# Kernel tuning notes

Hardware: AMD Instinct MI355X
Metric: run time of the kernel (lower is better)

The kernel has to match this reference:

```python
import jax, jax.numpy as jnp
import numpy as np
from jax import lax

BN_EPS = 1e-5


def _bn(t, g, b, m, v):
    # eval-mode BatchNorm2d over channel axis 1
    scale = (g / jnp.sqrt(v + BN_EPS))[None, :, None, None]
    return (t - m[None, :, None, None]) * scale + b[None, :, None, None]


def _conv1x1(t, w):
    # w: (out_c, in_c)
    return jnp.einsum('bchw,oc->bohw', t, w)


def setup_inputs() -> dict:
    key = jax.random.key(0)
    ks = jax.random.split(key, 8)
    B, C_in, H, W = 16, 640, 32, 32
    x = jax.random.normal(ks[0], (B, C_in, H, W), dtype=jnp.float32)

    def bn_params(k, c):
        k1, k2, k3, k4 = jax.random.split(k, 4)
        return (jax.random.normal(k1, (c,), jnp.float32) * 0.1 + 1.0,  # gamma
                jax.random.normal(k2, (c,), jnp.float32) * 0.1,        # beta
                jax.random.normal(k3, (c,), jnp.float32) * 0.1,        # running mean
                jax.random.uniform(k4, (c,), jnp.float32) + 0.5)       # running var

    bn1_g, bn1_b, bn1_m, bn1_v = bn_params(ks[1], 640)
    w_in = jax.random.normal(ks[2], (64, 640), jnp.float32) / np.sqrt(640)
    bnin_g, bnin_b, bnin_m, bnin_v = bn_params(ks[3], 64)
    w_emb = jax.random.normal(ks[4], (640, 1664), jnp.float32) / np.sqrt(1664)
    bne_g, bne_b, bne_m, bne_v = bn_params(ks[5], 640)
    w_out = jax.random.normal(ks[6], (640, 640), jnp.float32) / np.sqrt(640)
    bno_g, bno_b, bno_m, bno_v = bn_params(ks[7], 640)

    return dict(x=x,
                bn1_g=bn1_g, bn1_b=bn1_b, bn1_m=bn1_m, bn1_v=bn1_v,
                w_in=w_in, bnin_g=bnin_g, bnin_b=bnin_b, bnin_m=bnin_m, bnin_v=bnin_v,
                w_emb=w_emb, bne_g=bne_g, bne_b=bne_b, bne_m=bne_m, bne_v=bne_v,
                w_out=w_out, bno_g=bno_g, bno_b=bno_b, bno_m=bno_m, bno_v=bno_v)


def reference(x,
              bn1_g, bn1_b, bn1_m, bn1_v,
              w_in, bnin_g, bnin_b, bnin_m, bnin_v,
              w_emb, bne_g, bne_b, bne_m, bne_v,
              w_out, bno_g, bno_b, bno_m, bno_v):
    KH, KW = 5, 5
    x = jax.nn.relu(_bn(x, bn1_g, bn1_b, bn1_m, bn1_v))
    x = jax.nn.relu(_bn(_conv1x1(x, w_in), bnin_g, bnin_b, bnin_m, bnin_v))
    x0 = jax.nn.relu(x)  # second ReLU in original forward (no-op but faithful)
    # F.normalize(x, dim=1, p=2), eps=1e-12 (PyTorch default)
    norm = jnp.sqrt(jnp.sum(x0 * x0, axis=1, keepdims=True))
    identity = x0 / jnp.maximum(norm, 1e-12)
    b, c, h, w = identity.shape
    # unfold: (b, c*KH*KW, h, w), channel-major ordering matches torch Unfold
    patches = lax.conv_general_dilated_patches(
        identity, (KH, KW), (1, 1), ((2, 2), (2, 2)))
    corr = patches.reshape(b, c, KH * KW, h, w) * identity[:, :, None, :, :]
    corr = corr.reshape(b, c * KH * KW, h, w)
    # featureL2Norm: sqrt(sum(x^2, 1) + 1e-6)
    gs = corr / jnp.sqrt(jnp.sum(corr * corr, axis=1, keepdims=True) + 1e-6)
    feat = jnp.concatenate([identity, gs], axis=1)  # (b, 1664, h, w)
    e = jax.nn.relu(_bn(_conv1x1(feat, w_emb), bne_g, bne_b, bne_m, bne_v))
    out = _bn(_conv1x1(e, w_out), bno_g, bno_b, bno_m, bno_v)
    # dropout in eval mode = identity
    return out
```

## Files before the change

kernel.cpp:

```cpp
#include <hip/hip_runtime.h>
#include <math.h>

#define BN_EPS 1e-5f

using short8  = __attribute__((ext_vector_type(8))) short;
using f32x16  = __attribute__((ext_vector_type(16))) float;


__device__ __forceinline__ float bflo(unsigned u) { return __uint_as_float(u << 16); }
__device__ __forceinline__ float bfhi(unsigned u) { return __uint_as_float(u & 0xffff0000u); }

__device__ __forceinline__ unsigned bf16_rne(float f) {
    unsigned u = __float_as_uint(f);
    return (u + 0x7fffu + ((u >> 16) & 1u)) >> 16;
}
__device__ __forceinline__ unsigned pack_bf16(float lo, float hi) {
    return bf16_rne(lo) | (bf16_rne(hi) << 16);
}
__device__ __forceinline__ unsigned pk_hu(float lo, float hi) {
    unsigned a = __float_as_uint(lo) + 0x8000u;
    unsigned b = __float_as_uint(hi) + 0x8000u;
    return __builtin_amdgcn_perm(b, a, 0x07060302u);
}
__device__ __forceinline__ unsigned pmul_fast(unsigned a, unsigned b) {
    return pk_hu(bflo(a) * bflo(b), bfhi(a) * bfhi(b));
}

__global__ __launch_bounds__(256)
void k_prep(const float* __restrict__ g1, const float* __restrict__ b1,
            const float* __restrict__ m1, const float* __restrict__ v1,
            const float* __restrict__ w_in,
            const float* __restrict__ gi, const float* __restrict__ bi,
            const float* __restrict__ mi, const float* __restrict__ vi,
            const float* __restrict__ ge, const float* __restrict__ be,
            const float* __restrict__ me, const float* __restrict__ ve,
            const float* __restrict__ w_out,
            const float* __restrict__ go, const float* __restrict__ bo,
            const float* __restrict__ mo, const float* __restrict__ vo,
            float* __restrict__ s1, float* __restrict__ b1c,
            float* __restrict__ biasI, float* __restrict__ biasE, float* __restrict__ biasO,
            unsigned* __restrict__ wIt, unsigned* __restrict__ wOt)
{
    int i = blockIdx.x * 256 + threadIdx.x;

    if (i < 640) {
        float s = g1[i] * rsqrtf(v1[i] + BN_EPS);
        s1[i] = s; b1c[i] = b1[i] - m1[i] * s;
    } else if (i < 704) {
        int c = i - 640;
        float s = gi[c] * rsqrtf(vi[c] + BN_EPS);
        biasI[c] = bi[c] - mi[c] * s;
    } else if (i < 1344) {
        int c = i - 704;
        float s = ge[c] * rsqrtf(ve[c] + BN_EPS);
        biasE[c] = be[c] - me[c] * s;
    } else if (i < 1984) {
        int c = i - 1344;
        float s = go[c] * rsqrtf(vo[c] + BN_EPS);
        biasO[c] = bo[c] - mo[c] * s;
    }

    if (i >= 2048 && i < 7168) {
        int u = i - 2048;
        int kc = u >> 8, w = u & 255;
        int mf = w >> 7, kh = (w >> 6) & 1, sl = w & 63;
        int oc = mf * 32 + (sl & 31);
        int k0 = kc * 32 + kh * 16 + (sl >> 5) * 8;
        float sc = gi[oc] * rsqrtf(vi[oc] + BN_EPS);
        unsigned d[4];
#pragma unroll
        for (int q = 0; q < 4; q++)
            d[q] = pack_bf16(w_in[oc * 640 + k0 + 2 * q] * sc,
                             w_in[oc * 640 + k0 + 2 * q + 1] * sc);
        ((uint4*)wIt)[u] = make_uint4(d[0], d[1], d[2], d[3]);
    }

    if (i >= 8192 && i < 59392) {
        int u = i - 8192;
        int ci = u >> 9, w = u & 511;
        int mt = ci / 20, kc = ci - mt * 20;
        int mf = w >> 7, kh = (w >> 6) & 1, sl = w & 63;
        int oc = mt * 128 + mf * 32 + (sl & 31);
        int k0 = kc * 32 + kh * 16 + (sl >> 5) * 8;
        float sc = go[oc] * rsqrtf(vo[oc] + BN_EPS);
        unsigned d[4];
#pragma unroll
        for (int q = 0; q < 4; q++)
            d[q] = pack_bf16(w_out[oc * 640 + k0 + 2 * q] * sc,
                             w_out[oc * 640 + k0 + 2 * q + 1] * sc);
        ((uint4*)wOt)[u] = make_uint4(d[0], d[1], d[2], d[3]);
    }
}

__global__ __launch_bounds__(256)
void k_prepE(const float* __restrict__ w_emb,
             const float* __restrict__ ge, const float* __restrict__ ve,
             unsigned* __restrict__ wEt)
{
    __shared__ float row[1664];
    const int tid = threadIdx.x;
    const int oc = blockIdx.x;

#pragma unroll
    for (int it = 0; it < 2; it++) {
        int u = it * 256 + tid;
        if (u < 416)
            ((float4*)row)[u] = ((const float4*)&w_emb[(size_t)oc * 1664])[u];
    }
    __syncthreads();

    if (tid < 208) {
        int kc = tid >> 2, kh = (tid >> 1) & 1, ksub = tid & 1;
        int k0 = kc * 32 + kh * 16 + ksub * 8;
        float sc = ge[oc] * rsqrtf(ve[oc] + BN_EPS);
        float v[8];
#pragma unroll
        for (int j = 0; j < 8; j++) {
            int kgp = k0 + j;
            int orig;
            if (kgp < 64) orig = kgp;
            else { int t = kgp - 64; orig = 64 + (t & 63) * 25 + (t >> 6); }
            v[j] = row[orig] * sc;
        }
        int mt = oc >> 7, mf = (oc >> 5) & 3;
        int idx = (mt * 52 + kc) * 512 + (mf * 2 + kh) * 64 + ksub * 32 + (oc & 31);
        ((uint4*)wEt)[idx] = make_uint4(pack_bf16(v[0], v[1]), pack_bf16(v[2], v[3]),
                                        pack_bf16(v[4], v[5]), pack_bf16(v[6], v[7]));
    }
}

__global__ __launch_bounds__(256, 2)
void k_identity(const float* __restrict__ x,
                const float* __restrict__ s1, const float* __restrict__ b1c,
                const unsigned* __restrict__ wIt, const float* __restrict__ biasI,
                unsigned* __restrict__ ident)
{
    __shared__ short smem[4096];
    __shared__ float T[64 * 68];
    __shared__ float inv[64];

    const int tid = threadIdx.x;
    const int l = tid & 63, wv = tid >> 6;
    const int mf = wv >> 1, nf = wv & 1;
    const int p0 = blockIdx.x * 64;
    const int b = p0 >> 10, hw0 = p0 & 1023;

    f32x16 acc;
#pragma unroll
    for (int r = 0; r < 16; r++) acc[r] = 0.f;

    for (int kc = 0; kc < 20; kc++) {
        uint4 av = ((const uint4*)wIt)[kc * 256 + tid];
        int u = tid;
        int bnf = u >> 7, bkh = (u >> 6) & 1, sl = u & 63;
        int px = bnf * 32 + (sl & 31);
        int ch0 = kc * 32 + bkh * 16 + (sl >> 5) * 8;
        float4 sA = *(const float4*)&s1[ch0], sB = *(const float4*)&s1[ch0 + 4];
        float4 bA = *(const float4*)&b1c[ch0], bB = *(const float4*)&b1c[ch0 + 4];
        float vv[8];
        const float* xp = &x[((size_t)b * 640 + ch0) * 1024 + hw0 + px];
        vv[0] = fmaxf(fmaf(xp[0], sA.x, bA.x), 0.f);
        vv[1] = fmaxf(fmaf(xp[1024], sA.y, bA.y), 0.f);
        vv[2] = fmaxf(fmaf(xp[2048], sA.z, bA.z), 0.f);
        vv[3] = fmaxf(fmaf(xp[3072], sA.w, bA.w), 0.f);
        vv[4] = fmaxf(fmaf(xp[4096], sB.x, bB.x), 0.f);
        vv[5] = fmaxf(fmaf(xp[5120], sB.y, bB.y), 0.f);
        vv[6] = fmaxf(fmaf(xp[6144], sB.z, bB.z), 0.f);
        vv[7] = fmaxf(fmaf(xp[7168], sB.w, bB.w), 0.f);
        uint4 bvpk = make_uint4(pack_bf16(vv[0], vv[1]), pack_bf16(vv[2], vv[3]),
                                pack_bf16(vv[4], vv[5]), pack_bf16(vv[6], vv[7]));
        __syncthreads();
        ((uint4*)smem)[tid] = av;
        ((uint4*)(smem + 2048))[tid] = bvpk;
        __syncthreads();
#pragma unroll
        for (int kh = 0; kh < 2; kh++) {
            short8 a = *(const short8*)&smem[((mf * 2 + kh) * 64 + l) * 8];
            short8 bb = *(const short8*)&smem[2048 + ((nf * 2 + kh) * 64 + l) * 8];
            acc = __builtin_amdgcn_mfma_f32_32x32x16_bf16(a, bb, acc, 0, 0, 0);
        }
    }
    __syncthreads();
#pragma unroll
    for (int r = 0; r < 16; r++) {
        int m = mf * 32 + (r & 3) + 8 * (r >> 2) + 4 * (l >> 5);
        int px = nf * 32 + (l & 31);
        T[px * 68 + m] = fmaxf(acc[r] + biasI[m], 0.f);
    }
    __syncthreads();
    if (tid < 64) {
        float sum = 0.f;
#pragma unroll 8
        for (int c = 0; c < 64; c++) { float v = T[tid * 68 + c]; sum = fmaf(v, v, sum); }
        inv[tid] = 1.f / fmaxf(sqrtf(sum), 1e-12f);
    }
    __syncthreads();
    {
        int px = tid >> 2, q = tid & 3;
        float iv = inv[px];
        unsigned d[8];
#pragma unroll
        for (int t = 0; t < 8; t++)
            d[t] = pack_bf16(T[px * 68 + q * 16 + 2 * t] * iv, T[px * 68 + q * 16 + 2 * t + 1] * iv);
        uint4* dst = (uint4*)&ident[((size_t)(p0 + px) * 64 + q * 16) / 2];
        dst[0] = make_uint4(d[0], d[1], d[2], d[3]);
        dst[1] = make_uint4(d[4], d[5], d[6], d[7]);
    }
}

#define FS_SLAB 0
#define FS_CTRS 15552
__global__ __launch_bounds__(256, 3)
void k_feat(const unsigned* __restrict__ ident, unsigned* __restrict__ featC, int ptBase)
{
    __shared__ short smem[20160];
    __shared__ float invDs[64];

    const int tid = threadIdx.x;
    const int pt = ptBase + blockIdx.x;
    const int b = pt >> 4, r0 = (pt & 15) * 2;

#pragma unroll
    for (int it = 0; it < 7; it++) {
        int u = it * 256 + tid;
        if (u < 1728) {
            int spx = u >> 3, q = u & 7;
            int sr = spx / 36, sc = spx - sr * 36;
            int r = r0 + sr - 2, c = sc - 2;
            uint4 v = make_uint4(0u, 0u, 0u, 0u);
            if (r >= 0 && r < 32 && c >= 0 && c < 32)
                v = *(const uint4*)&ident[((size_t)(b * 1024 + r * 32 + c) * 64 + q * 8) / 2];
            *(uint4*)&smem[FS_SLAB + spx * 72 + q * 8] = v;
        }
    }
    __syncthreads();

    {
        int px = tid >> 2, part = tid & 3;
        int rh = px >> 5, rw = px & 31;
        float ctr[16];
        const unsigned* cp = (const unsigned*)&smem[FS_SLAB + ((rh + 2) * 36 + rw + 2) * 72 + part * 16];
#pragma unroll
        for (int d = 0; d < 8; d++) { ctr[2 * d] = bflo(cp[d]); ctr[2 * d + 1] = bfhi(cp[d]); }
        float sum = 0.f;
#pragma unroll
        for (int k = 0; k < 25; k++) {
            const int kh = k / 5, kw = k % 5;
            const unsigned* nb = (const unsigned*)&smem[FS_SLAB + ((rh + kh) * 36 + rw + kw) * 72 + part * 16];
#pragma unroll
            for (int d = 0; d < 8; d++) {
                float q0 = bflo(nb[d]) * ctr[2 * d];
                float q1 = bfhi(nb[d]) * ctr[2 * d + 1];
                sum = fmaf(q0, q0, sum); sum = fmaf(q1, q1, sum);
            }
        }
        sum += __shfl_xor(sum, 1);
        sum += __shfl_xor(sum, 2);
        if (part == 0) invDs[px] = rsqrtf(sum + 1e-6f);
    }
    __syncthreads();

#pragma unroll
    for (int it = 0; it < 2; it++) {
        int u = it * 256 + tid;
        int px = u >> 3, q = u & 7;
        int spx = ((px >> 5) + 2) * 36 + (px & 31) + 2;
        const unsigned* src = (const unsigned*)&smem[FS_SLAB + spx * 72 + q * 8];
        float iv = invDs[px];
        unsigned d[4];
#pragma unroll
        for (int dd = 0; dd < 4; dd++)
            d[dd] = pk_hu(bflo(src[dd]) * iv, bfhi(src[dd]) * iv);
        *(uint4*)&smem[FS_CTRS + px * 72 + q * 8] = make_uint4(d[0], d[1], d[2], d[3]);
    }
    __syncthreads();

    const int hf = tid >> 7, bkh = (tid >> 6) & 1, sl = tid & 63;
    const int pxl = hf * 32 + (sl & 31);
    const int cl = bkh * 16 + (sl >> 5) * 8;
    const int spxC = (hf + 2) * 36 + (sl & 31) + 2;
    uint4* dst = (uint4*)featC + (size_t)blockIdx.x * 52 * 256 + tid;

    for (int kc = 0; kc < 52; kc++) {
        uint4 f;
        if (kc < 2) {
            f = *(const uint4*)&smem[FS_SLAB + spxC * 72 + kc * 32 + cl];
        } else {
            int idx = kc - 2;
            int ksp = idx >> 1;
            int cb = (idx & 1) * 32 + cl;
            int kho = ksp / 5, kwo = ksp - kho * 5;
            int spx = (hf + kho) * 36 + (sl & 31) + kwo;
            const unsigned* nb = (const unsigned*)&smem[FS_SLAB + spx * 72 + cb];
            const unsigned* ct = (const unsigned*)&smem[FS_CTRS + pxl * 72 + cb];
            f = make_uint4(pmul_fast(nb[0], ct[0]), pmul_fast(nb[1], ct[1]),
                           pmul_fast(nb[2], ct[2]), pmul_fast(nb[3], ct[3]));
        }
        dst[kc * 256] = f;
    }
}

__global__ __launch_bounds__(256, 4)
void k_emb(const unsigned* __restrict__ featC, const unsigned* __restrict__ wEt,
           const float* __restrict__ biasE, unsigned* __restrict__ eG, int ntBase)
{
    __shared__ short Ep[128 * 136];

    const int tid = threadIdx.x;
    const int l = tid & 63, wv = tid >> 6;
    const int mh = wv >> 1, nh = wv & 1;
    const int ntL = blockIdx.x, mt = blockIdx.y;

    f32x16 acc[2][2];
#pragma unroll
    for (int i = 0; i < 2; i++)
#pragma unroll
        for (int j = 0; j < 2; j++)
#pragma unroll
            for (int r = 0; r < 16; r++) acc[i][j][r] = 0.f;

    const uint4* A = (const uint4*)wEt + (size_t)(mt * 52) * 512;
    const uint4* B = (const uint4*)featC + (size_t)ntL * 2 * 52 * 256;

    for (int kc = 0; kc < 52; kc++) {
        uint4 av[2][2], bv[2][2];
#pragma unroll
        for (int mi = 0; mi < 2; mi++)
#pragma unroll
            for (int kh = 0; kh < 2; kh++)
                av[mi][kh] = A[(size_t)kc * 512 + ((mh * 2 + mi) * 2 + kh) * 64 + l];
#pragma unroll
        for (int ni = 0; ni < 2; ni++) {
            int bnf = 2 * nh + ni;
#pragma unroll
            for (int kh = 0; kh < 2; kh++)
                bv[ni][kh] = B[((size_t)(bnf >> 1) * 52 + kc) * 256 + ((bnf & 1) << 7) + (kh << 6) + l];
        }
#pragma unroll
        for (int kh = 0; kh < 2; kh++) {
            acc[0][0] = __builtin_amdgcn_mfma_f32_32x32x16_bf16(*(short8*)&av[0][kh], *(short8*)&bv[0][kh], acc[0][0], 0, 0, 0);
            acc[0][1] = __builtin_amdgcn_mfma_f32_32x32x16_bf16(*(short8*)&av[0][kh], *(short8*)&bv[1][kh], acc[0][1], 0, 0, 0);
            acc[1][0] = __builtin_amdgcn_mfma_f32_32x32x16_bf16(*(short8*)&av[1][kh], *(short8*)&bv[0][kh], acc[1][0], 0, 0, 0);
            acc[1][1] = __builtin_amdgcn_mfma_f32_32x32x16_bf16(*(short8*)&av[1][kh], *(short8*)&bv[1][kh], acc[1][1], 0, 0, 0);
        }
    }

#pragma unroll
    for (int mi = 0; mi < 2; mi++)
#pragma unroll
        for (int ni = 0; ni < 2; ni++) {
            int px = (nh * 2 + ni) * 32 + (l & 31);
#pragma unroll
            for (int r = 0; r < 16; r += 2) {
                int m = (mh * 2 + mi) * 32 + (r & 3) + 8 * (r >> 2) + 4 * (l >> 5);
                float v0 = fmaxf(acc[mi][ni][r] + biasE[mt * 128 + m], 0.f);
                float v1 = fmaxf(acc[mi][ni][r + 1] + biasE[mt * 128 + m + 1], 0.f);
                *(unsigned*)&Ep[px * 136 + m] = pack_bf16(v0, v1);
            }
        }
    __syncthreads();
#pragma unroll
    for (int it = 0; it < 8; it++) {
        int w = it * 256 + tid;
        int oct = w >> 7, pxl = w & 127;
        uint4 v = *(const uint4*)&Ep[pxl * 136 + oct * 8];
        int kcp = mt * 4 + (oct >> 2);
        int bkh = (oct >> 1) & 1, ksub = oct & 1;
        int ptg = (ntBase + ntL) * 2 + (pxl >> 6);
        int hf = (pxl >> 5) & 1, sl2 = ksub * 32 + (pxl & 31);
        ((uint4*)eG)[((size_t)ptg * 20 + kcp) * 256 + (hf << 7) + (bkh << 6) + sl2] = v;
    }
}

__global__ __launch_bounds__(256, 4)
void k_out(const unsigned* __restrict__ eG, const unsigned* __restrict__ wOt,
           const float* __restrict__ biasO, float* __restrict__ out)
{
    const int tid = threadIdx.x;
    const int l = tid & 63, wv = tid >> 6;
    const int mh = wv >> 1, nh = wv & 1;
    const int nt = blockIdx.x, mt = blockIdx.y;
    const int p0 = nt * 128;
    const int b = p0 >> 10, hw0 = p0 & 1023;

    f32x16 acc[2][2];
#pragma unroll
    for (int i = 0; i < 2; i++)
#pragma unroll
        for (int j = 0; j < 2; j++)
#pragma unroll
            for (int r = 0; r < 16; r++) acc[i][j][r] = 0.f;

    const uint4* A = (const uint4*)wOt + (size_t)(mt * 20) * 512;
    const uint4* B = (const uint4*)eG + (size_t)nt * 2 * 20 * 256;

    for (int kc = 0; kc < 20; kc++) {
        uint4 av[2][2], bv[2][2];
#pragma unroll
        for (int mi = 0; mi < 2; mi++)
#pragma unroll
            for (int kh = 0; kh < 2; kh++)
                av[mi][kh] = A[(size_t)kc * 512 + ((mh * 2 + mi) * 2 + kh) * 64 + l];
#pragma unroll
        for (int ni = 0; ni < 2; ni++) {
            int bnf = 2 * nh + ni;
#pragma unroll
            for (int kh = 0; kh < 2; kh++)
                bv[ni][kh] = B[((size_t)(bnf >> 1) * 20 + kc) * 256 + ((bnf & 1) << 7) + (kh << 6) + l];
        }
#pragma unroll
        for (int kh = 0; kh < 2; kh++) {
            acc[0][0] = __builtin_amdgcn_mfma_f32_32x32x16_bf16(*(short8*)&av[0][kh], *(short8*)&bv[0][kh], acc[0][0], 0, 0, 0);
            acc[0][1] = __builtin_amdgcn_mfma_f32_32x32x16_bf16(*(short8*)&av[0][kh], *(short8*)&bv[1][kh], acc[0][1], 0, 0, 0);
            acc[1][0] = __builtin_amdgcn_mfma_f32_32x32x16_bf16(*(short8*)&av[1][kh], *(short8*)&bv[0][kh], acc[1][0], 0, 0, 0);
            acc[1][1] = __builtin_amdgcn_mfma_f32_32x32x16_bf16(*(short8*)&av[1][kh], *(short8*)&bv[1][kh], acc[1][1], 0, 0, 0);
        }
    }
#pragma unroll
    for (int mi = 0; mi < 2; mi++)
#pragma unroll
        for (int ni = 0; ni < 2; ni++) {
            int pxl = (nh * 2 + ni) * 32 + (l & 31);
#pragma unroll
            for (int r = 0; r < 16; r++) {
                int oc = mt * 128 + (mh * 2 + mi) * 32 + (r & 3) + 8 * (r >> 2) + 4 * (l >> 5);
                out[((size_t)b * 640 + oc) * 1024 + hw0 + pxl] = acc[mi][ni][r] + biasO[oc];
            }
        }
}

extern "C" void kernel_launch(void* const* d_in, const int* in_sizes, int n_in,
                              void* d_out, int out_size, void* d_ws, size_t ws_size,
                              hipStream_t stream)
{
    const float* x    = (const float*)d_in[0];
    const float* g1   = (const float*)d_in[1];
    const float* b1   = (const float*)d_in[2];
    const float* m1   = (const float*)d_in[3];
    const float* v1   = (const float*)d_in[4];
    const float* w_in = (const float*)d_in[5];
    const float* gi   = (const float*)d_in[6];
    const float* bi   = (const float*)d_in[7];
    const float* mi   = (const float*)d_in[8];
    const float* vi   = (const float*)d_in[9];
    const float* w_emb= (const float*)d_in[10];
    const float* ge   = (const float*)d_in[11];
    const float* be   = (const float*)d_in[12];
    const float* me   = (const float*)d_in[13];
    const float* ve   = (const float*)d_in[14];
    const float* w_out= (const float*)d_in[15];
    const float* go   = (const float*)d_in[16];
    const float* bo   = (const float*)d_in[17];
    const float* mo   = (const float*)d_in[18];
    const float* vo   = (const float*)d_in[19];

    char* ws = (char*)d_ws;
    float*    s1    = (float*)(ws + 0);
    float*    b1c   = (float*)(ws + 2560);
    float*    biasI = (float*)(ws + 5120);
    float*    biasE = (float*)(ws + 5376);
    float*    biasO = (float*)(ws + 7936);
    unsigned* wIt   = (unsigned*)(ws + 16384);
    unsigned* wOt   = (unsigned*)(ws + 98304);
    unsigned* wEt   = (unsigned*)(ws + 917504);
    unsigned* ident = (unsigned*)(ws + 3047424);
    unsigned* eG    = (unsigned*)(ws + 5144576);
    float*    out   = (float*)d_out;

    const size_t featFullOff = 26116096ull;
    const size_t featFullBytes = 256ull * 52 * 256 * 16;

    k_prep<<<232, 256, 0, stream>>>(g1, b1, m1, v1, w_in, gi, bi, mi, vi,
                                    ge, be, me, ve, w_out, go, bo, mo, vo,
                                    s1, b1c, biasI, biasE, biasO, wIt, wOt);
    k_prepE<<<640, 256, 0, stream>>>(w_emb, ge, ve, wEt);
    k_identity<<<256, 256, 0, stream>>>(x, s1, b1c, wIt, biasI, ident);

    if (ws_size >= featFullOff + featFullBytes) {
        unsigned* featC = (unsigned*)(ws + featFullOff);
        k_feat<<<256, 256, 0, stream>>>(ident, featC, 0);
        k_emb<<<dim3(128, 5), 256, 0, stream>>>(featC, wEt, biasE, eG, 0);
    } else {
        unsigned* featC = (unsigned*)(ws + 16384);
        for (int c = 0; c < 64; c++) {
            k_feat<<<4, 256, 0, stream>>>(ident, featC, c * 4);
            k_emb<<<dim3(2, 5), 256, 0, stream>>>(featC, wEt, biasE, eG, c * 2);
        }
        k_prep<<<232, 256, 0, stream>>>(g1, b1, m1, v1, w_in, gi, bi, mi, vi,
                                        ge, be, me, ve, w_out, go, bo, mo, vo,
                                        s1, b1c, biasI, biasE, biasO, wIt, wOt);
    }
    k_out<<<dim3(128, 5), 256, 0, stream>>>(eG, wOt, biasO, out);
}
```

Before: 231.1 us.

## Split K across 512-thread blocks and double-buffer register fragments in GEMMs

k_identity and k_feat now run with 512 threads per block. k_identity splits the 640-channel reduction across two halves and merges the partial sums through shared memory. k_feat spreads the norm computation and the feature packing over twice as many threads. The k_emb and k_out GEMM loops now prefetch the next k-chunk's fragments into a second register set, so global loads overlap the MFMA work, and their launch bounds drop from 4 to 2 waves per SIMD. This trades occupancy and extra registers for more latency hiding per wave.

```diff
diff --git a/kernel.cpp b/kernel.cpp
--- a/kernel.cpp
+++ b/kernel.cpp
@@ -129,18 +129,21 @@
     }
 }
 
-__global__ __launch_bounds__(256, 2)
+__global__ __launch_bounds__(512, 1)
 void k_identity(const float* __restrict__ x,
                 const float* __restrict__ s1, const float* __restrict__ b1c,
                 const unsigned* __restrict__ wIt, const float* __restrict__ biasI,
                 unsigned* __restrict__ ident)
 {
-    __shared__ short smem[4096];
+    __shared__ short smem[2][4096];
+    __shared__ float Tpart[64 * 65];
     __shared__ float T[64 * 68];
     __shared__ float inv[64];
 
-    const int tid = threadIdx.x;
-    const int l = tid & 63, wv = tid >> 6;
+    const int tid  = threadIdx.x;
+    const int half = tid >> 8;
+    const int t    = tid & 255;
+    const int l = t & 63, wv = t >> 6;
     const int mf = wv >> 1, nf = wv & 1;
     const int p0 = blockIdx.x * 64;
     const int b = p0 >> 10, hw0 = p0 & 1023;
@@ -149,10 +152,10 @@
 #pragma unroll
     for (int r = 0; r < 16; r++) acc[r] = 0.f;
 
-    for (int kc = 0; kc < 20; kc++) {
-        uint4 av = ((const uint4*)wIt)[kc * 256 + tid];
-        int u = tid;
-        int bnf = u >> 7, bkh = (u >> 6) & 1, sl = u & 63;
+    for (int i = 0; i < 10; i++) {
+        const int kc = half * 10 + i;
+        uint4 av = ((const uint4*)wIt)[kc * 256 + t];
+        int bnf = t >> 7, bkh = (t >> 6) & 1, sl = t & 63;
         int px = bnf * 32 + (sl & 31);
         int ch0 = kc * 32 + bkh * 16 + (sl >> 5) * 8;
         float4 sA = *(const float4*)&s1[ch0], sB = *(const float4*)&s1[ch0 + 4];
@@ -170,22 +173,33 @@
         uint4 bvpk = make_uint4(pack_bf16(vv[0], vv[1]), pack_bf16(vv[2], vv[3]),
                                 pack_bf16(vv[4], vv[5]), pack_bf16(vv[6], vv[7]));
         __syncthreads();
-        ((uint4*)smem)[tid] = av;
-        ((uint4*)(smem + 2048))[tid] = bvpk;
+        ((uint4*)smem[half])[t] = av;
+        ((uint4*)(smem[half] + 2048))[t] = bvpk;
         __syncthreads();
 #pragma unroll
         for (int kh = 0; kh < 2; kh++) {
-            short8 a = *(const short8*)&smem[((mf * 2 + kh) * 64 + l) * 8];
-            short8 bb = *(const short8*)&smem[2048 + ((nf * 2 + kh) * 64 + l) * 8];
+            short8 a  = *(const short8*)&smem[half][((mf * 2 + kh) * 64 + l) * 8];
+            short8 bb = *(const short8*)&smem[half][2048 + ((nf * 2 + kh) * 64 + l) * 8];
             acc = __builtin_amdgcn_mfma_f32_32x32x16_bf16(a, bb, acc, 0, 0, 0);
         }
     }
-    __syncthreads();
-#pragma unroll
-    for (int r = 0; r < 16; r++) {
-        int m = mf * 32 + (r & 3) + 8 * (r >> 2) + 4 * (l >> 5);
-        int px = nf * 32 + (l & 31);
-        T[px * 68 + m] = fmaxf(acc[r] + biasI[m], 0.f);
+    if (half == 1) {
+#pragma unroll
+        for (int r = 0; r < 16; r++) {
+            int m = mf * 32 + (r & 3) + 8 * (r >> 2) + 4 * (l >> 5);
+            int px = nf * 32 + (l & 31);
+            Tpart[px * 65 + m] = acc[r];
+        }
+    }
+    __syncthreads();
+    if (half == 0) {
+#pragma unroll
+        for (int r = 0; r < 16; r++) {
+            int m = mf * 32 + (r & 3) + 8 * (r >> 2) + 4 * (l >> 5);
+            int px = nf * 32 + (l & 31);
+            float v = acc[r] + Tpart[px * 65 + m];
+            T[px * 68 + m] = fmaxf(v + biasI[m], 0.f);
+        }
     }
     __syncthreads();
     if (tid < 64) {
@@ -196,21 +210,20 @@
     }
     __syncthreads();
     {
-        int px = tid >> 2, q = tid & 3;
+        int px = tid >> 3, q = tid & 7;
         float iv = inv[px];
-        unsigned d[8];
-#pragma unroll
-        for (int t = 0; t < 8; t++)
-            d[t] = pack_bf16(T[px * 68 + q * 16 + 2 * t] * iv, T[px * 68 + q * 16 + 2 * t + 1] * iv);
-        uint4* dst = (uint4*)&ident[((size_t)(p0 + px) * 64 + q * 16) / 2];
-        dst[0] = make_uint4(d[0], d[1], d[2], d[3]);
-        dst[1] = make_uint4(d[4], d[5], d[6], d[7]);
+        unsigned d[4];
+#pragma unroll
+        for (int t2 = 0; t2 < 4; t2++)
+            d[t2] = pack_bf16(T[px * 68 + q * 8 + 2 * t2] * iv,
+                              T[px * 68 + q * 8 + 2 * t2 + 1] * iv);
+        *(uint4*)&ident[(size_t)(p0 + px) * 32 + q * 4] = make_uint4(d[0], d[1], d[2], d[3]);
     }
 }
 
 #define FS_SLAB 0
 #define FS_CTRS 15552
-__global__ __launch_bounds__(256, 3)
+__global__ __launch_bounds__(512, 1)
 void k_feat(const unsigned* __restrict__ ident, unsigned* __restrict__ featC, int ptBase)
 {
     __shared__ short smem[20160];
@@ -221,8 +234,8 @@
     const int b = pt >> 4, r0 = (pt & 15) * 2;
 
 #pragma unroll
-    for (int it = 0; it < 7; it++) {
-        int u = it * 256 + tid;
+    for (int it = 0; it < 4; it++) {
+        int u = it * 512 + tid;
         if (u < 1728) {
             int spx = u >> 3, q = u & 7;
             int sr = spx / 36, sc = spx - sr * 36;
@@ -236,19 +249,19 @@
     __syncthreads();
 
     {
-        int px = tid >> 2, part = tid & 3;
+        int px = tid >> 3, part = tid & 7;
         int rh = px >> 5, rw = px & 31;
-        float ctr[16];
-        const unsigned* cp = (const unsigned*)&smem[FS_SLAB + ((rh + 2) * 36 + rw + 2) * 72 + part * 16];
-#pragma unroll
-        for (int d = 0; d < 8; d++) { ctr[2 * d] = bflo(cp[d]); ctr[2 * d + 1] = bfhi(cp[d]); }
+        float ctr[8];
+        const unsigned* cp = (const unsigned*)&smem[FS_SLAB + ((rh + 2) * 36 + rw + 2) * 72 + part * 8];
+#pragma unroll
+        for (int d = 0; d < 4; d++) { ctr[2 * d] = bflo(cp[d]); ctr[2 * d + 1] = bfhi(cp[d]); }
         float sum = 0.f;
 #pragma unroll
         for (int k = 0; k < 25; k++) {
             const int kh = k / 5, kw = k % 5;
-            const unsigned* nb = (const unsigned*)&smem[FS_SLAB + ((rh + kh) * 36 + rw + kw) * 72 + part * 16];
-#pragma unroll
-            for (int d = 0; d < 8; d++) {
+            const unsigned* nb = (const unsigned*)&smem[FS_SLAB + ((rh + kh) * 36 + rw + kw) * 72 + part * 8];
+#pragma unroll
+            for (int d = 0; d < 4; d++) {
                 float q0 = bflo(nb[d]) * ctr[2 * d];
                 float q1 = bfhi(nb[d]) * ctr[2 * d + 1];
                 sum = fmaf(q0, q0, sum); sum = fmaf(q1, q1, sum);
@@ -256,14 +269,13 @@
         }
         sum += __shfl_xor(sum, 1);
         sum += __shfl_xor(sum, 2);
+        sum += __shfl_xor(sum, 4);
         if (part == 0) invDs[px] = rsqrtf(sum + 1e-6f);
     }
     __syncthreads();
 
-#pragma unroll
-    for (int it = 0; it < 2; it++) {
-        int u = it * 256 + tid;
-        int px = u >> 3, q = u & 7;
+    {
+        int px = tid >> 3, q = tid & 7;
         int spx = ((px >> 5) + 2) * 36 + (px & 31) + 2;
         const unsigned* src = (const unsigned*)&smem[FS_SLAB + spx * 72 + q * 8];
         float iv = invDs[px];
@@ -275,13 +287,16 @@
     }
     __syncthreads();
 
-    const int hf = tid >> 7, bkh = (tid >> 6) & 1, sl = tid & 63;
+    const int t = tid & 255;
+    const int hf = t >> 7, bkh = (t >> 6) & 1, sl = t & 63;
     const int pxl = hf * 32 + (sl & 31);
     const int cl = bkh * 16 + (sl >> 5) * 8;
     const int spxC = (hf + 2) * 36 + (sl & 31) + 2;
-    uint4* dst = (uint4*)featC + (size_t)blockIdx.x * 52 * 256 + tid;
-
-    for (int kc = 0; kc < 52; kc++) {
+    const int kcH = tid >> 8;
+    uint4* dst = (uint4*)featC + (size_t)blockIdx.x * 52 * 256 + t;
+
+    for (int it = 0; it < 26; it++) {
+        int kc = it * 2 + kcH;
         uint4 f;
         if (kc < 2) {
             f = *(const uint4*)&smem[FS_SLAB + spxC * 72 + kc * 32 + cl];
@@ -300,7 +315,35 @@
     }
 }
 
-__global__ __launch_bounds__(256, 4)
+__device__ __forceinline__ void ld_frag(const uint4* __restrict__ A, const uint4* __restrict__ B,
+                                        int kc, int mh, int nh, int l,
+                                        uint4 av[2][2], uint4 bv[2][2])
+{
+#pragma unroll
+    for (int mi = 0; mi < 2; mi++)
+#pragma unroll
+        for (int kh = 0; kh < 2; kh++)
+            av[mi][kh] = A[(size_t)kc * 512 + ((mh * 2 + mi) * 2 + kh) * 64 + l];
+#pragma unroll
+    for (int ni = 0; ni < 2; ni++) {
+        int bnf = 2 * nh + ni;
+#pragma unroll
+        for (int kh = 0; kh < 2; kh++)
+            bv[ni][kh] = B[((size_t)(bnf >> 1) * 52 + kc) * 256 + ((bnf & 1) << 7) + (kh << 6) + l];
+    }
+}
+__device__ __forceinline__ void do_mfma(uint4 av[2][2], uint4 bv[2][2], f32x16 acc[2][2])
+{
+#pragma unroll
+    for (int kh = 0; kh < 2; kh++) {
+        acc[0][0] = __builtin_amdgcn_mfma_f32_32x32x16_bf16(*(short8*)&av[0][kh], *(short8*)&bv[0][kh], acc[0][0], 0, 0, 0);
+        acc[0][1] = __builtin_amdgcn_mfma_f32_32x32x16_bf16(*(short8*)&av[0][kh], *(short8*)&bv[1][kh], acc[0][1], 0, 0, 0);
+        acc[1][0] = __builtin_amdgcn_mfma_f32_32x32x16_bf16(*(short8*)&av[1][kh], *(short8*)&bv[0][kh], acc[1][0], 0, 0, 0);
+        acc[1][1] = __builtin_amdgcn_mfma_f32_32x32x16_bf16(*(short8*)&av[1][kh], *(short8*)&bv[1][kh], acc[1][1], 0, 0, 0);
+    }
+}
+
+__global__ __launch_bounds__(256, 2)
 void k_emb(const unsigned* __restrict__ featC, const unsigned* __restrict__ wEt,
            const float* __restrict__ biasE, unsigned* __restrict__ eG, int ntBase)
 {
@@ -322,27 +365,13 @@
     const uint4* A = (const uint4*)wEt + (size_t)(mt * 52) * 512;
     const uint4* B = (const uint4*)featC + (size_t)ntL * 2 * 52 * 256;
 
-    for (int kc = 0; kc < 52; kc++) {
-        uint4 av[2][2], bv[2][2];
-#pragma unroll
-        for (int mi = 0; mi < 2; mi++)
-#pragma unroll
-            for (int kh = 0; kh < 2; kh++)
-                av[mi][kh] = A[(size_t)kc * 512 + ((mh * 2 + mi) * 2 + kh) * 64 + l];
-#pragma unroll
-        for (int ni = 0; ni < 2; ni++) {
-            int bnf = 2 * nh + ni;
-#pragma unroll
-            for (int kh = 0; kh < 2; kh++)
-                bv[ni][kh] = B[((size_t)(bnf >> 1) * 52 + kc) * 256 + ((bnf & 1) << 7) + (kh << 6) + l];
-        }
-#pragma unroll
-        for (int kh = 0; kh < 2; kh++) {
-            acc[0][0] = __builtin_amdgcn_mfma_f32_32x32x16_bf16(*(short8*)&av[0][kh], *(short8*)&bv[0][kh], acc[0][0], 0, 0, 0);
-            acc[0][1] = __builtin_amdgcn_mfma_f32_32x32x16_bf16(*(short8*)&av[0][kh], *(short8*)&bv[1][kh], acc[0][1], 0, 0, 0);
-            acc[1][0] = __builtin_amdgcn_mfma_f32_32x32x16_bf16(*(short8*)&av[1][kh], *(short8*)&bv[0][kh], acc[1][0], 0, 0, 0);
-            acc[1][1] = __builtin_amdgcn_mfma_f32_32x32x16_bf16(*(short8*)&av[1][kh], *(short8*)&bv[1][kh], acc[1][1], 0, 0, 0);
-        }
+    uint4 a0[2][2], b0[2][2], a1[2][2], b1[2][2];
+    ld_frag(A, B, 0, mh, nh, l, a0, b0);
+    for (int kc = 0; kc < 52; kc += 2) {
+        ld_frag(A, B, kc + 1, mh, nh, l, a1, b1);
+        do_mfma(a0, b0, acc);
+        if (kc + 2 < 52) ld_frag(A, B, kc + 2, mh, nh, l, a0, b0);
+        do_mfma(a1, b1, acc);
     }
 
 #pragma unroll
@@ -372,7 +401,25 @@
     }
 }
 
-__global__ __launch_bounds__(256, 4)
+__device__ __forceinline__ void ld_fragO(const uint4* __restrict__ A, const uint4* __restrict__ B,
+                                         int kc, int mh, int nh, int l,
+                                         uint4 av[2][2], uint4 bv[2][2])
+{
+#pragma unroll
+    for (int mi = 0; mi < 2; mi++)
+#pragma unroll
+        for (int kh = 0; kh < 2; kh++)
+            av[mi][kh] = A[(size_t)kc * 512 + ((mh * 2 + mi) * 2 + kh) * 64 + l];
+#pragma unroll
+    for (int ni = 0; ni < 2; ni++) {
+        int bnf = 2 * nh + ni;
+#pragma unroll
+        for (int kh = 0; kh < 2; kh++)
+            bv[ni][kh] = B[((size_t)(bnf >> 1) * 20 + kc) * 256 + ((bnf & 1) << 7) + (kh << 6) + l];
+    }
+}
+
+__global__ __launch_bounds__(256, 2)
 void k_out(const unsigned* __restrict__ eG, const unsigned* __restrict__ wOt,
            const float* __restrict__ biasO, float* __restrict__ out)
 {
@@ -394,27 +441,13 @@
     const uint4* A = (const uint4*)wOt + (size_t)(mt * 20) * 512;
     const uint4* B = (const uint4*)eG + (size_t)nt * 2 * 20 * 256;
 
-    for (int kc = 0; kc < 20; kc++) {
-        uint4 av[2][2], bv[2][2];
-#pragma unroll
-        for (int mi = 0; mi < 2; mi++)
-#pragma unroll
-            for (int kh = 0; kh < 2; kh++)
-                av[mi][kh] = A[(size_t)kc * 512 + ((mh * 2 + mi) * 2 + kh) * 64 + l];
-#pragma unroll
-        for (int ni = 0; ni < 2; ni++) {
-            int bnf = 2 * nh + ni;
-#pragma unroll
-            for (int kh = 0; kh < 2; kh++)
-                bv[ni][kh] = B[((size_t)(bnf >> 1) * 20 + kc) * 256 + ((bnf & 1) << 7) + (kh << 6) + l];
-        }
-#pragma unroll
-        for (int kh = 0; kh < 2; kh++) {
-            acc[0][0] = __builtin_amdgcn_mfma_f32_32x32x16_bf16(*(short8*)&av[0][kh], *(short8*)&bv[0][kh], acc[0][0], 0, 0, 0);
-            acc[0][1] = __builtin_amdgcn_mfma_f32_32x32x16_bf16(*(short8*)&av[0][kh], *(short8*)&bv[1][kh], acc[0][1], 0, 0, 0);
-            acc[1][0] = __builtin_amdgcn_mfma_f32_32x32x16_bf16(*(short8*)&av[1][kh], *(short8*)&bv[0][kh], acc[1][0], 0, 0, 0);
-            acc[1][1] = __builtin_amdgcn_mfma_f32_32x32x16_bf16(*(short8*)&av[1][kh], *(short8*)&bv[1][kh], acc[1][1], 0, 0, 0);
-        }
+    uint4 a0[2][2], b0[2][2], a1[2][2], b1[2][2];
+    ld_fragO(A, B, 0, mh, nh, l, a0, b0);
+    for (int kc = 0; kc < 20; kc += 2) {
+        ld_fragO(A, B, kc + 1, mh, nh, l, a1, b1);
+        do_mfma(a0, b0, acc);
+        if (kc + 2 < 20) ld_fragO(A, B, kc + 2, mh, nh, l, a0, b0);
+        do_mfma(a1, b1, acc);
     }
 #pragma unroll
     for (int mi = 0; mi < 2; mi++)
@@ -474,16 +507,16 @@
                                     ge, be, me, ve, w_out, go, bo, mo, vo,
                                     s1, b1c, biasI, biasE, biasO, wIt, wOt);
     k_prepE<<<640, 256, 0, stream>>>(w_emb, ge, ve, wEt);
-    k_identity<<<256, 256, 0, stream>>>(x, s1, b1c, wIt, biasI, ident);
+    k_identity<<<256, 512, 0, stream>>>(x, s1, b1c, wIt, biasI, ident);
 
     if (ws_size >= featFullOff + featFullBytes) {
         unsigned* featC = (unsigned*)(ws + featFullOff);
-        k_feat<<<256, 256, 0, stream>>>(ident, featC, 0);
+        k_feat<<<256, 512, 0, stream>>>(ident, featC, 0);
         k_emb<<<dim3(128, 5), 256, 0, stream>>>(featC, wEt, biasE, eG, 0);
     } else {
         unsigned* featC = (unsigned*)(ws + 16384);
         for (int c = 0; c < 64; c++) {
-            k_feat<<<4, 256, 0, stream>>>(ident, featC, c * 4);
+            k_feat<<<4, 512, 0, stream>>>(ident, featC, c * 4);
             k_emb<<<dim3(2, 5), 256, 0, stream>>>(featC, wEt, biasE, eG, c * 2);
         }
         k_prep<<<232, 256, 0, stream>>>(g1, b1, m1, v1, w_in, gi, bi, mi, vi,
```

After: 230.5 us. About the same (-0.2%).
